# Performance work log

Measured on AMD Instinct MI355X. Metric: run time of the kernel, lower is better.

## Reference

```python
import jax, jax.numpy as jnp
import numpy as np

B, H, N, L = 8, 128, 64, 8192
LOG_DT_MIN, LOG_DT_MAX = float(np.log(0.001)), float(np.log(0.1))


def setup_inputs() -> dict:
    key = jax.random.key(0)
    k_x, k_are, k_aim, k_c, k_dt = jax.random.split(key, 5)
    x = jax.random.normal(k_x, (B, H, L), dtype=jnp.float32)
    # A_re: negative real parts (clipped to <= -1e-4 in forward anyway)
    A_re = -jax.random.uniform(k_are, (H, N, 1), dtype=jnp.float32, minval=0.1, maxval=1.0)
    A_im = jax.random.normal(k_aim, (H, N, 1), dtype=jnp.float32) * float(np.pi)
    C = (0.5 ** 0.5) * jax.random.normal(k_c, (H, N, 2), dtype=jnp.float32)
    D = jnp.ones((1, H, 1), dtype=jnp.float32)
    u = jax.random.uniform(k_dt, (H, 1, 1), dtype=jnp.float32)
    log_delta = u * (LOG_DT_MAX - LOG_DT_MIN) + LOG_DT_MIN
    return {"x": x, "A_re": A_re, "A_im": A_im, "C": C, "D": D, "log_delta": log_delta}


def reference(x, A_re, A_im, C, D, log_delta):
    seq_len = x.shape[-1]
    # ---- S4D-ZOH kernel generation ----
    A = jnp.minimum(A_re, -1e-4) + 1j * A_im            # (H, N, 1) complex
    Cc = C[..., 0:1] + 1j * C[..., 1:2]                 # (H, N, 1) complex
    step = jnp.exp(log_delta)                           # (H, 1, 1)
    dA = step * A                                       # (H, N, 1)
    times = jnp.arange(seq_len, dtype=jnp.float32)[None, None, :]  # (1, 1, L)
    part = jnp.exp(times * dA)                          # (H, N, L)
    cons = (jnp.exp(dA) - 1.0) / A                      # (H, N, 1)
    K = jnp.sum(Cc * cons * part, axis=-2).real         # (H, L)
    # ---- causal conv via FFT (torch pads both to length 2L) ----
    n = seq_len + K.shape[-1]                           # 2L
    xd = jnp.fft.rfft(x, n=n, axis=-1)                  # (B, H, L+1)
    Kd = jnp.fft.rfft(K[None], n=n, axis=-1)            # (1, H, L+1)
    conv = jnp.fft.irfft(xd * Kd, n=n, axis=-1)[:, :, :seq_len]
    return conv + D * x
```

## Files before the change

### kernel.cpp

```cpp
#include <hip/hip_runtime.h>
#include <hip/hip_bf16.h>
#include <math.h>

#define B_ 8
#define H_ 128
#define N_ 64
#define L_ 8192
#define MCH 64
#define SCH (L_ / MCH)
#define EROW 136

#define LDS_TBL   34816
#define LDS_SEG   51200
#define LDS_KV    53248
#define LDS_TOTAL 53504

typedef __attribute__((ext_vector_type(8))) short bf16x8;
typedef __attribute__((ext_vector_type(4))) float f32x4;

__device__ __forceinline__ float bf2f(ushort s) { return __uint_as_float(((uint)s) << 16); }
__device__ __forceinline__ uint packbf2(float a, float b) {
    __hip_bfloat162 h = __float22bfloat162_rn(make_float2(a, b));
    union { __hip_bfloat162 h2; uint u; } cv; cv.h2 = h;
    return cv.u;
}
__device__ __forceinline__ bf16x8 pack_bf8(f32x4 a, f32x4 b) {
    union { uint u[4]; bf16x8 v; } r;
    r.u[0] = packbf2(a[0], a[1]); r.u[1] = packbf2(a[2], a[3]);
    r.u[2] = packbf2(b[0], b[1]); r.u[3] = packbf2(b[2], b[3]);
    return r.v;
}

__global__ __launch_bounds__(256, 3) void s4d_fused(
    const float* __restrict__ x,
    const float* __restrict__ A_re, const float* __restrict__ A_im,
    const float* __restrict__ Cp, const float* __restrict__ Dp,
    const float* __restrict__ log_delta,
    float* __restrict__ out)
{
    __shared__ __align__(16) char lds[LDS_TOTAL];
    ushort* EBUF  = (ushort*)lds;
    float*  kpart = (float*)lds;
    char*   TBLb  = lds + LDS_TBL;
    float*  segr  = (float*)(lds + LDS_SEG);
    float*  segi  = segr + 256;
    float*  kv    = (float*)(lds + LDS_KV);

    const int seq = blockIdx.x;
    const int h   = seq % H_;
    const int tid = threadIdx.x;
    const int w   = tid >> 6;
    const int lane = tid & 63;
    const int n16 = lane & 15, q = lane >> 4;
    const int n = tid & 63;
    const int g = tid >> 6;

    float are = fminf(A_re[h * N_ + n], -1e-4f);
    float aim = A_im[h * N_ + n];
    float step = expf(log_delta[h]);
    float dre = step * are, dim = step * aim;
    float er = expf(dre);
    float sd, cd; sincosf(dim, &sd, &cd);
    float rre = er * cd, rim = er * sd;
    float cre = Cp[(h * N_ + n) * 2 + 0];
    float cim = Cp[(h * N_ + n) * 2 + 1];
    float inv  = 1.0f / (are * are + aim * aim);
    float numr = rre - 1.0f, numi = rim;
    float consr = (numr * are + numi * aim) * inv;
    float consi = (numi * are - numr * aim) * inv;
    float wr = cre * consr - cim * consi;
    float wi = cre * consi + cim * consr;
    float dval = Dp[h];
    float m64r = rre, m64i = rim;
#pragma unroll
    for (int k = 0; k < 6; ++k) { float tr = m64r*m64r - m64i*m64i, ti = 2.f*m64r*m64i; m64r = tr; m64i = ti; }

    auto rp = [&](float d, float& pr, float& pi) {
        float ex = __expf(d * dre);
        float ang = d * dim;
        float s = __sinf(ang), c2 = __cosf(ang);
        pr = ex * c2; pi = ex * s;
    };

    const float* xs = x + (size_t)seq * L_;
    bf16x8 xbv[2][2];
#pragma unroll
    for (int ic = 0; ic < 2; ++ic) {
        int c = (2 * w + ic) * 16 + n16;
#pragma unroll
        for (int kc = 0; kc < 2; ++kc) {
            const float* p = xs + c * MCH + kc * 32 + q * 8;
            f32x4 f0 = __builtin_nontemporal_load((const f32x4*)p);
            f32x4 f1 = __builtin_nontemporal_load((const f32x4*)p + 1);
            xbv[ic][kc] = pack_bf8(f0, f1);
        }
    }

#pragma unroll
    for (int j = 0; j < 16; ++j) {
        int d = g * 16 + j;
        float pr, pi; rp((float)d, pr, pi);
        kpart[d * 65 + n] = wr * pr - wi * pi;
    }
    __syncthreads();
    if (tid < 64) {
        float s = 0.f;
#pragma unroll
        for (int m = 0; m < 64; ++m) s += kpart[tid * 65 + m];
        kv[tid] = s;
    }
    __syncthreads();

    {
        uint tw[8];
#pragma unroll
        for (int i = 0; i < 8; ++i) {
            int t0 = g * 16 + 2 * i, t1 = t0 + 1;
            float v0 = (t0 <= n) ? kv[n - t0] : 0.f;
            float v1 = (t1 <= n) ? kv[n - t1] : 0.f;
            if (t0 == n) v0 += dval;
            if (t1 == n) v1 += dval;
            tw[i] = packbf2(v0, v1);
        }
        const uint xt = (uint)(n & 7) << 4;
        *(uint4*)(TBLb + ((n * 128 + g * 32     ) ^ xt)) = ((uint4*)tw)[0];
        *(uint4*)(TBLb + ((n * 128 + g * 32 + 16) ^ xt)) = ((uint4*)tw)[1];
    }
    __syncthreads();

    const uint xr = (uint)(n16 & 7) << 4;
    f32x4 accT[4][2];
#pragma unroll
    for (int rt = 0; rt < 4; ++rt) {
        int row = rt * 16 + n16;
        bf16x8 t0 = *(const bf16x8*)(TBLb + ((row * 128      + q * 16) ^ xr));
        bf16x8 t1 = *(const bf16x8*)(TBLb + ((row * 128 + 64 + q * 16) ^ xr));
#pragma unroll
        for (int ic = 0; ic < 2; ++ic) {
            f32x4 a = {0.f, 0.f, 0.f, 0.f};
            a = __builtin_amdgcn_mfma_f32_16x16x32_bf16(t0, xbv[ic][0], a, 0, 0, 0);
            a = __builtin_amdgcn_mfma_f32_16x16x32_bf16(t1, xbv[ic][1], a, 0, 0, 0);
            accT[rt][ic] = a;
        }
    }
    __syncthreads();

    {
        uint qr[8], qi[8];
#pragma unroll
        for (int i = 0; i < 8; ++i) {
            int t0 = g * 16 + 2 * i;
            float ar0, ai0, ar1, ai1;
            rp((float)(63 - t0), ar0, ai0);
            rp((float)(62 - t0), ar1, ai1);
            qr[i] = packbf2(ar0, ar1);
            qi[i] = packbf2(ai0, ai1);
        }
        const int ra = 2 * n, rb = 2 * n + 1;
        const uint xa = (uint)(ra & 7) << 4, xbm = (uint)(rb & 7) << 4;
        *(uint4*)(TBLb + ((ra * 128 + g * 32     ) ^ xa)) = ((uint4*)qr)[0];
        *(uint4*)(TBLb + ((ra * 128 + g * 32 + 16) ^ xa)) = ((uint4*)qr)[1];
        *(uint4*)(TBLb + ((rb * 128 + g * 32     ) ^ xbm)) = ((uint4*)qi)[0];
        *(uint4*)(TBLb + ((rb * 128 + g * 32 + 16) ^ xbm)) = ((uint4*)qi)[1];
    }
    __syncthreads();

#pragma unroll
    for (int rt = 0; rt < 8; ++rt) {
        int row = rt * 16 + n16;
        bf16x8 a0 = *(const bf16x8*)(TBLb + ((row * 128      + q * 16) ^ xr));
        bf16x8 a1 = *(const bf16x8*)(TBLb + ((row * 128 + 64 + q * 16) ^ xr));
#pragma unroll
        for (int ic = 0; ic < 2; ++ic) {
            f32x4 acc = {0.f, 0.f, 0.f, 0.f};
            acc = __builtin_amdgcn_mfma_f32_16x16x32_bf16(a0, xbv[ic][0], acc, 0, 0, 0);
            acc = __builtin_amdgcn_mfma_f32_16x16x32_bf16(a1, xbv[ic][1], acc, 0, 0, 0);
            int c = (2 * w + ic) * 16 + n16;
            uint2 st = make_uint2(packbf2(acc[0], acc[1]), packbf2(acc[2], acc[3]));
            *(uint2*)&EBUF[c * EROW + rt * 16 + q * 4] = st;
        }
    }
    __syncthreads();

    float mr = m64r, mi = m64i;
    float m32r = mr, m32i = mi;
#pragma unroll
    for (int k = 0; k < 5; ++k) {
        float tr = m32r * m32r - m32i * m32i, ti = 2.f * m32r * m32i;
        m32r = tr; m32i = ti;
    }
    {
        float sr = 0.f, si = 0.f;
#pragma unroll
        for (int j = 0; j < 32; ++j) {
            uint e = *(const uint*)&EBUF[(g * 32 + j) * EROW + 2 * n];
            float er2 = bf2f((ushort)(e & 0xffffu)), ei2 = bf2f((ushort)(e >> 16));
            float nr = er2 + mr * sr - mi * si;
            float ni = ei2 + mr * si + mi * sr;
            sr = nr; si = ni;
        }
        segr[g * 64 + n] = sr; segi[g * 64 + n] = si;
    }
    {
#pragma unroll
        for (int i = 0; i < 16; ++i) {
            int j = g * 16 + i;
            float pr, pi; rp((float)(j + 1), pr, pi);
            float ur = wr * pr - wi * pi;
            float ui = wr * pi + wi * pr;
            *(uint*)(TBLb + ((j * 256 + n * 4) ^ ((uint)(j & 7) << 4))) = packbf2(ur, -ui);
        }
    }
    __syncthreads();
    {
        float pr2 = 0.f, pi2 = 0.f;
        for (int gp = 0; gp < g; ++gp) {
            float Er = segr[gp * 64 + n], Ei = segi[gp * 64 + n];
            float nr = Er + m32r * pr2 - m32i * pi2;
            float ni = Ei + m32r * pi2 + m32i * pr2;
            pr2 = nr; pi2 = ni;
        }
        float sr = pr2, si = pi2;
#pragma unroll
        for (int j = 0; j < 32; ++j) {
            uint* ep = (uint*)&EBUF[(g * 32 + j) * EROW + 2 * n];
            uint e = *ep;
            float er2 = bf2f((ushort)(e & 0xffffu)), ei2 = bf2f((ushort)(e >> 16));
            *ep = packbf2(sr, si);
            float nr = er2 + mr * sr - mi * si;
            float ni = ei2 + mr * si + mi * sr;
            sr = nr; si = ni;
        }
    }
    __syncthreads();

    float* op = out + (size_t)seq * L_;
#pragma unroll
    for (int rt = 0; rt < 4; ++rt) {
        int row = rt * 16 + n16;
        bf16x8 p0 = *(const bf16x8*)(TBLb + ((row * 256       + q * 16) ^ xr));
        bf16x8 p1 = *(const bf16x8*)(TBLb + ((row * 256 +  64 + q * 16) ^ xr));
        bf16x8 p2 = *(const bf16x8*)(TBLb + ((row * 256 + 128 + q * 16) ^ xr));
        bf16x8 p3 = *(const bf16x8*)(TBLb + ((row * 256 + 192 + q * 16) ^ xr));
#pragma unroll
        for (int ic = 0; ic < 2; ++ic) {
            int c = (2 * w + ic) * 16 + n16;
            f32x4 accP = {0.f, 0.f, 0.f, 0.f};
            accP = __builtin_amdgcn_mfma_f32_16x16x32_bf16(p0,
                       *(const bf16x8*)&EBUF[c * EROW +       q * 8], accP, 0, 0, 0);
            accP = __builtin_amdgcn_mfma_f32_16x16x32_bf16(p1,
                       *(const bf16x8*)&EBUF[c * EROW +  32 + q * 8], accP, 0, 0, 0);
            accP = __builtin_amdgcn_mfma_f32_16x16x32_bf16(p2,
                       *(const bf16x8*)&EBUF[c * EROW +  64 + q * 8], accP, 0, 0, 0);
            accP = __builtin_amdgcn_mfma_f32_16x16x32_bf16(p3,
                       *(const bf16x8*)&EBUF[c * EROW +  96 + q * 8], accP, 0, 0, 0);
            f32x4 o;
            o[0] = accT[rt][ic][0] + accP[0];
            o[1] = accT[rt][ic][1] + accP[1];
            o[2] = accT[rt][ic][2] + accP[2];
            o[3] = accT[rt][ic][3] + accP[3];
            __builtin_nontemporal_store(o, (f32x4*)(op + c * MCH + rt * 16 + q * 4));
        }
    }
}

extern "C" void kernel_launch(void* const* d_in, const int* in_sizes, int n_in,
                              void* d_out, int out_size, void* d_ws, size_t ws_size,
                              hipStream_t stream)
{
    const float* x  = (const float*)d_in[0];
    const float* Ar = (const float*)d_in[1];
    const float* Ai = (const float*)d_in[2];
    const float* C  = (const float*)d_in[3];
    const float* D  = (const float*)d_in[4];
    const float* ld = (const float*)d_in[5];
    float* out = (float*)d_out;
    (void)d_ws; (void)ws_size;

    hipLaunchKernelGGL(s4d_fused, dim3(B_ * H_), dim3(256), 0, stream,
                       x, Ar, Ai, C, D, ld, out);
}
```

Before: 112.9 us.

## Replace LDS kernel reduction with wave shuffles and build Toeplitz fragments in registers

```diff
diff --git a/kernel.cpp b/kernel.cpp
--- a/kernel.cpp
+++ b/kernel.cpp
@@ -40,7 +40,6 @@
 {
     __shared__ __align__(16) char lds[LDS_TOTAL];
     ushort* EBUF  = (ushort*)lds;
-    float*  kpart = (float*)lds;
     char*   TBLb  = lds + LDS_TBL;
     float*  segr  = (float*)(lds + LDS_SEG);
     float*  segi  = segr + 256;
@@ -52,8 +51,8 @@
     const int w   = tid >> 6;
     const int lane = tid & 63;
     const int n16 = lane & 15, q = lane >> 4;
-    const int n = tid & 63;
-    const int g = tid >> 6;
+    const int n = lane;
+    const int g = w;
 
     float are = fminf(A_re[h * N_ + n], -1e-4f);
     float aim = A_im[h * N_ + n];
@@ -96,55 +95,6 @@
         }
     }
 
-#pragma unroll
-    for (int j = 0; j < 16; ++j) {
-        int d = g * 16 + j;
-        float pr, pi; rp((float)d, pr, pi);
-        kpart[d * 65 + n] = wr * pr - wi * pi;
-    }
-    __syncthreads();
-    if (tid < 64) {
-        float s = 0.f;
-#pragma unroll
-        for (int m = 0; m < 64; ++m) s += kpart[tid * 65 + m];
-        kv[tid] = s;
-    }
-    __syncthreads();
-
-    {
-        uint tw[8];
-#pragma unroll
-        for (int i = 0; i < 8; ++i) {
-            int t0 = g * 16 + 2 * i, t1 = t0 + 1;
-            float v0 = (t0 <= n) ? kv[n - t0] : 0.f;
-            float v1 = (t1 <= n) ? kv[n - t1] : 0.f;
-            if (t0 == n) v0 += dval;
-            if (t1 == n) v1 += dval;
-            tw[i] = packbf2(v0, v1);
-        }
-        const uint xt = (uint)(n & 7) << 4;
-        *(uint4*)(TBLb + ((n * 128 + g * 32     ) ^ xt)) = ((uint4*)tw)[0];
-        *(uint4*)(TBLb + ((n * 128 + g * 32 + 16) ^ xt)) = ((uint4*)tw)[1];
-    }
-    __syncthreads();
-
-    const uint xr = (uint)(n16 & 7) << 4;
-    f32x4 accT[4][2];
-#pragma unroll
-    for (int rt = 0; rt < 4; ++rt) {
-        int row = rt * 16 + n16;
-        bf16x8 t0 = *(const bf16x8*)(TBLb + ((row * 128      + q * 16) ^ xr));
-        bf16x8 t1 = *(const bf16x8*)(TBLb + ((row * 128 + 64 + q * 16) ^ xr));
-#pragma unroll
-        for (int ic = 0; ic < 2; ++ic) {
-            f32x4 a = {0.f, 0.f, 0.f, 0.f};
-            a = __builtin_amdgcn_mfma_f32_16x16x32_bf16(t0, xbv[ic][0], a, 0, 0, 0);
-            a = __builtin_amdgcn_mfma_f32_16x16x32_bf16(t1, xbv[ic][1], a, 0, 0, 0);
-            accT[rt][ic] = a;
-        }
-    }
-    __syncthreads();
-
     {
         uint qr[8], qi[8];
 #pragma unroll
@@ -163,8 +113,27 @@
         *(uint4*)(TBLb + ((rb * 128 + g * 32     ) ^ xbm)) = ((uint4*)qi)[0];
         *(uint4*)(TBLb + ((rb * 128 + g * 32 + 16) ^ xbm)) = ((uint4*)qi)[1];
     }
+
+    {
+        float kvloc[16];
+#pragma unroll
+        for (int j = 0; j < 16; ++j) {
+            float pr, pi; rp((float)(g * 16 + j), pr, pi);
+            kvloc[j] = wr * pr - wi * pi;
+        }
+#pragma unroll
+        for (int j = 0; j < 16; ++j) {
+#pragma unroll
+            for (int s = 1; s < 64; s <<= 1)
+                kvloc[j] += __shfl_xor(kvloc[j], s, 64);
+        }
+#pragma unroll
+        for (int j = 0; j < 16; ++j)
+            if (n == j) kv[g * 16 + j] = kvloc[j];
+    }
     __syncthreads();
 
+    const uint xr = (uint)(n16 & 7) << 4;
 #pragma unroll
     for (int rt = 0; rt < 8; ++rt) {
         int row = rt * 16 + n16;
@@ -180,7 +149,6 @@
             *(uint2*)&EBUF[c * EROW + rt * 16 + q * 4] = st;
         }
     }
-    __syncthreads();
 
     float mr = m64r, mi = m64i;
     float m32r = mr, m32i = mi;
@@ -189,6 +157,7 @@
         float tr = m32r * m32r - m32i * m32i, ti = 2.f * m32r * m32i;
         m32r = tr; m32i = ti;
     }
+
     {
         float sr = 0.f, si = 0.f;
 #pragma unroll
@@ -201,17 +170,42 @@
         }
         segr[g * 64 + n] = sr; segi[g * 64 + n] = si;
     }
-    {
-#pragma unroll
-        for (int i = 0; i < 16; ++i) {
-            int j = g * 16 + i;
-            float pr, pi; rp((float)(j + 1), pr, pi);
-            float ur = wr * pr - wi * pi;
-            float ui = wr * pi + wi * pr;
-            *(uint*)(TBLb + ((j * 256 + n * 4) ^ ((uint)(j & 7) << 4))) = packbf2(ur, -ui);
+
+    f32x4 accT[4][2];
+#pragma unroll
+    for (int rt = 0; rt < 4; ++rt) {
+        int row = rt * 16 + n16;
+        union { uint u[4]; bf16x8 v; } f0, f1;
+#pragma unroll
+        for (int kc = 0; kc < 2; ++kc) {
+#pragma unroll
+            for (int ki = 0; ki < 4; ++ki) {
+                int t0 = kc * 32 + q * 8 + 2 * ki;
+                int i0 = row - t0, i1 = i0 - 1;
+                float v0 = kv[i0 & 63]; v0 = (i0 >= 0) ? v0 : 0.f; if (i0 == 0) v0 += dval;
+                float v1 = kv[i1 & 63]; v1 = (i1 >= 0) ? v1 : 0.f; if (i1 == 0) v1 += dval;
+                if (kc == 0) f0.u[ki] = packbf2(v0, v1); else f1.u[ki] = packbf2(v0, v1);
+            }
+        }
+#pragma unroll
+        for (int ic = 0; ic < 2; ++ic) {
+            f32x4 a = {0.f, 0.f, 0.f, 0.f};
+            a = __builtin_amdgcn_mfma_f32_16x16x32_bf16(f0.v, xbv[ic][0], a, 0, 0, 0);
+            a = __builtin_amdgcn_mfma_f32_16x16x32_bf16(f1.v, xbv[ic][1], a, 0, 0, 0);
+            accT[rt][ic] = a;
         }
     }
     __syncthreads();
+
+#pragma unroll
+    for (int i = 0; i < 16; ++i) {
+        int j = g * 16 + i;
+        float pr, pi; rp((float)(j + 1), pr, pi);
+        float ur = wr * pr - wi * pi;
+        float ui = wr * pi + wi * pr;
+        *(uint*)(TBLb + ((j * 256 + n * 4) ^ ((uint)(j & 7) << 4))) = packbf2(ur, -ui);
+    }
+
     {
         float pr2 = 0.f, pi2 = 0.f;
         for (int gp = 0; gp < g; ++gp) {
```

After: 109.0 us. 3.5% less time.
